# Kernel optimization log

Hardware: AMD Instinct MI355X
Metric: run time of the kernel (lower is better)

The kernel has to match this reference:

```python
import jax, jax.numpy as jnp
import numpy as np

NUM_LAYERS = 4
D_MODEL = 1024
N_HEAD = 8
HEAD_DIM = D_MODEL // N_HEAD
FFN_DIM = 4096
B, L = 8, 512
LN_EPS = 1e-5


def rel_pos_embed(seq_len, dim, init_size=1200, padding_idx=0):
    # RelativeSinusoidalPositionalEmbedding.get_embedding(init_size+1, dim, 0)
    num = init_size + 1  # 1201
    half = dim // 2
    inv = np.exp(np.arange(half, dtype=np.float64) * -(np.log(10000.0) / (half - 1)))
    pos = np.arange(-num // 2, num // 2, dtype=np.float64)[:, None] * inv[None, :]
    emb = np.concatenate([np.sin(pos), np.cos(pos)], axis=1)  # [num, dim]
    emb[padding_idx] = 0.0
    origin_shift = num // 2 + 1  # 601
    idx = np.arange(-seq_len, seq_len) + origin_shift  # [2L]
    return jnp.asarray(emb[idx], dtype=jnp.float32)  # [2L, dim]


def _shift(BD):
    # [b,h,L,2L] -> [b,h,L,L], selecting relative offsets k-q
    b, h, l, _ = BD.shape
    BD = jnp.concatenate([BD, jnp.zeros((b, h, l, 1), BD.dtype)], axis=-1)
    BD = BD.reshape(b, h, -1, l)[:, :, :-1].reshape(b, h, l, 2 * l)
    return BD[:, :, :, l:]


def _transpose_shift(E):
    # [b,h,L,2L] -> [b,h,L,L]
    b, h, l, _ = E.shape
    E = jnp.concatenate([E, jnp.zeros((b, h, l, 1), E.dtype)], axis=-1)
    E = E.reshape(b, h, 2 * l + 1, l)
    E = E[:, :, 2 * jnp.arange(l) + 1, :]  # [b,h,L,L]
    return jnp.swapaxes(E, -1, -2)


def layer_norm(x, g, b):
    mu = x.mean(-1, keepdims=True)
    var = ((x - mu) ** 2).mean(-1, keepdims=True)
    return (x - mu) / jnp.sqrt(var + LN_EPS) * g + b


def rel_attn(x, mask, qkv_w, r_r, r_w, pos):
    bsz, l, d = x.shape
    qkv = x @ qkv_w  # [b,L,3D]
    q, k, v = jnp.split(qkv, 3, axis=-1)
    to_heads = lambda t: t.reshape(bsz, l, N_HEAD, HEAD_DIM).transpose(0, 2, 1, 3)
    q, k, v = to_heads(q), to_heads(k), to_heads(v)  # [b,h,L,hd]
    rw_q = q + r_r[:, None]  # (original adds r_r_bias here)
    AC = jnp.einsum('bnqd,bnkd->bnqk', rw_q, k)
    D_ = jnp.einsum('nd,ld->nl', r_w, pos)[None, :, None]   # [1,h,1,2L]
    B_ = jnp.einsum('bnqd,ld->bnql', q, pos)                # [b,h,L,2L]
    E_ = jnp.einsum('bnqd,ld->bnql', k, pos)
    BDE = _shift(B_ + D_) + _transpose_shift(E_)
    attn = AC + BDE  # scale == 1 (scale=False)
    attn = jnp.where(mask[:, None, None, :] == 0, -jnp.inf, attn)
    attn = jax.nn.softmax(attn, axis=-1)
    out = jnp.einsum('bnqk,bnkd->bnqd', attn, v)
    return out.transpose(0, 2, 1, 3).reshape(bsz, l, d)


def setup_inputs() -> dict:
    key = jax.random.key(0)
    ks = jax.random.split(key, 12)
    Ln = NUM_LAYERS
    s = 0.02
    return {
        'x': jax.random.normal(ks[0], (B, L, D_MODEL), jnp.float32),
        'mask': jnp.ones((B, L), jnp.int32),
        'qkv_w': jax.random.normal(ks[1], (Ln, D_MODEL, 3 * D_MODEL), jnp.float32) * s,
        'r_r_bias': jax.random.normal(ks[2], (Ln, N_HEAD, HEAD_DIM), jnp.float32) * s,
        'r_w_bias': jax.random.normal(ks[3], (Ln, N_HEAD, HEAD_DIM), jnp.float32) * s,
        'ln1_g': jnp.ones((Ln, D_MODEL), jnp.float32),
        'ln1_b': jnp.zeros((Ln, D_MODEL), jnp.float32),
        'ln2_g': jnp.ones((Ln, D_MODEL), jnp.float32),
        'ln2_b': jnp.zeros((Ln, D_MODEL), jnp.float32),
        'w1': jax.random.normal(ks[4], (Ln, D_MODEL, FFN_DIM), jnp.float32) * s,
        'b1': jnp.zeros((Ln, FFN_DIM), jnp.float32),
        'w2': jax.random.normal(ks[5], (Ln, FFN_DIM, D_MODEL), jnp.float32) * s,
        'b2': jnp.zeros((Ln, D_MODEL), jnp.float32),
    }


def reference(x, mask, qkv_w, r_r_bias, r_w_bias, ln1_g, ln1_b, ln2_g, ln2_b, w1, b1, w2, b2):
    pos = rel_pos_embed(x.shape[1], HEAD_DIM)  # [2L, hd], buffer (detached)
    for i in range(NUM_LAYERS):  # after_norm=True (post-LN)
        a = rel_attn(x, mask, qkv_w[i], r_r_bias[i], r_w_bias[i], pos)
        x = layer_norm(x + a, ln1_g[i], ln1_b[i])
        h = jax.nn.relu(x @ w1[i] + b1[i]) @ w2[i] + b2[i]
        x = layer_norm(x + h, ln2_g[i], ln2_b[i])
    return x
```

## Files before the change

kernel.cpp:

```cpp
#include <hip/hip_runtime.h>

#define SEQ 512
#define DM 1024
#define NH 8
#define HD 128
#define FFN 4096
#define NL 4
#define NB 8

typedef __attribute__((ext_vector_type(8))) _Float16 half8v;
typedef __attribute__((ext_vector_type(8))) unsigned short ushort8v;
typedef __attribute__((ext_vector_type(4))) float float4v;

__device__ __forceinline__ unsigned short f2h(float f) {
  _Float16 h = (_Float16)f;
  return *(unsigned short*)&h;
}
__device__ __forceinline__ float h2f(unsigned short u) {
  _Float16 h = *(_Float16*)&u;
  return (float)h;
}

__global__ void sc_kernel(float* __restrict__ sc) {
  int idx = blockIdx.x * blockDim.x + threadIdx.x;
  int q = idx >> 6, c = idx & 63;
  if (q >= SEQ) return;
  double a = exp(-(double)c * (9.210340371976184 / 63.0));
  double p = (double)q * a;
  sc[q * 128 + c] = (float)sin(p);
  sc[q * 128 + 64 + c] = (float)cos(p);
}

__global__ void cvt_copy(const float* __restrict__ in, float* __restrict__ xout,
                         unsigned short* __restrict__ xh, int n4) {
  int i = blockIdx.x * blockDim.x + threadIdx.x;
  if (i >= n4) return;
  float4 v = ((const float4*)in)[i];
  ((float4*)xout)[i] = v;
  ushort4 u;
  u.x = f2h(v.x); u.y = f2h(v.y); u.z = f2h(v.z); u.w = f2h(v.w);
  ((ushort4*)xh)[i] = u;
}

__global__ __launch_bounds__(256) void transpose_cvt(
    const float* __restrict__ in, unsigned short* __restrict__ out, int K, int N) {
  __shared__ float t[32][33];
  int n0 = blockIdx.x * 32, k0 = blockIdx.y * 32;
  int c = threadIdx.x & 31, r = threadIdx.x >> 5;
#pragma unroll
  for (int i = 0; i < 32; i += 8)
    t[r + i][c] = in[(long long)(k0 + r + i) * N + n0 + c];
  __syncthreads();
#pragma unroll
  for (int i = 0; i < 32; i += 8)
    out[(long long)(n0 + r + i) * K + k0 + c] = f2h(t[c][r + i]);
}

template<int R>
__device__ __forceinline__ void stage_tile(
    const unsigned short* __restrict__ g, long long ld, int k0,
    unsigned short* lds, int tid) {
#pragma unroll
  for (int i = 0; i < R / 32; i++) {
    int p = i * 256 + tid;
    int row = p >> 3, cs = p & 7;
    int c = cs ^ (row & 7);
    const unsigned short* src = g + (long long)row * ld + k0 + c * 8;
    __builtin_amdgcn_global_load_lds(
        (const __attribute__((address_space(1))) void*)src,
        (__attribute__((address_space(3))) void*)(lds + p * 8),
        16, 0, 0);
  }
}

template<int BIAS, int RELU, int OUTH, int NF, int DBUF>
__global__ __launch_bounds__(256) void gemm_mfma(
    const unsigned short* __restrict__ A, int lda,
    const unsigned short* __restrict__ Bt, int ldb,
    const float* __restrict__ bias,
    void* __restrict__ Cv, int ldc,
    int K) {
  const int BN = 32 * NF;
  __shared__ __align__(16) unsigned short Asm[DBUF + 1][128 * 64];
  __shared__ __align__(16) unsigned short Bsm[DBUF + 1][BN * 64];
  const int tid = threadIdx.x, lane = tid & 63, wave = tid >> 6;
  const int wr = wave >> 1, wc = wave & 1;
  int nwg = gridDim.x * gridDim.y;
  int lin = blockIdx.y * gridDim.x + blockIdx.x;
  int swz = (lin & 7) * (nwg >> 3) + (lin >> 3);
  int bx = swz % gridDim.x, by = swz / gridDim.x;
  const unsigned short* Ag = A + (long long)by * 128 * lda;
  const unsigned short* Bg = Bt + (long long)bx * BN * ldb;
  const int l15 = lane & 15, l4 = lane >> 4;
  float4v acc[4][NF] = {};
  if (DBUF) {
    stage_tile<128>(Ag, lda, 0, Asm[0], tid);
    stage_tile<BN>(Bg, ldb, 0, Bsm[0], tid);
  }
  int cur = 0;
  for (int k0 = 0; k0 < K; k0 += 64) {
    if (DBUF) {
      __syncthreads();
      if (k0 + 64 < K) {
        stage_tile<128>(Ag, lda, k0 + 64, Asm[cur ^ 1], tid);
        stage_tile<BN>(Bg, ldb, k0 + 64, Bsm[cur ^ 1], tid);
      }
    } else {
      __syncthreads();
      stage_tile<128>(Ag, lda, k0, Asm[0], tid);
      stage_tile<BN>(Bg, ldb, k0, Bsm[0], tid);
      __syncthreads();
    }
#pragma unroll
    for (int kk = 0; kk < 2; kk++) {
      half8v af[4], bf[NF];
#pragma unroll
      for (int m = 0; m < 4; m++) {
        int row = wr * 64 + m * 16 + l15;
        int cs = (kk * 4 + l4) ^ (row & 7);
        af[m] = *(const half8v*)&Asm[cur][row * 64 + cs * 8];
      }
#pragma unroll
      for (int n = 0; n < NF; n++) {
        int row = wc * 16 * NF + n * 16 + l15;
        int cs = (kk * 4 + l4) ^ (row & 7);
        bf[n] = *(const half8v*)&Bsm[cur][row * 64 + cs * 8];
      }
#pragma unroll
      for (int m = 0; m < 4; m++)
#pragma unroll
        for (int n = 0; n < NF; n++)
          acc[m][n] = __builtin_amdgcn_mfma_f32_16x16x32_f16(af[m], bf[n], acc[m][n], 0, 0, 0);
    }
    if (DBUF) cur ^= 1;
  }
#pragma unroll
  for (int n = 0; n < NF; n++) {
    int ccol = bx * BN + wc * 16 * NF + n * 16 + l15;
    float bv = BIAS ? bias[ccol] : 0.f;
#pragma unroll
    for (int m = 0; m < 4; m++) {
      int crow0 = by * 128 + wr * 64 + m * 16 + l4 * 4;
#pragma unroll
      for (int j = 0; j < 4; j++) {
        float v = acc[m][n][j] + bv;
        if (RELU) v = fmaxf(v, 0.f);
        long long off = (long long)(crow0 + j) * ldc + ccol;
        if (OUTH) ((unsigned short*)Cv)[off] = f2h(v);
        else      ((float*)Cv)[off] = v;
      }
    }
  }
}

template<int OUTH, int ZSH, int NF, int DBUF>
__global__ __launch_bounds__(256) void gemm_bat(
    const unsigned short* __restrict__ A, int lda, long long sAz,
    const unsigned short* __restrict__ Bt, int ldb, long long sBz,
    void* __restrict__ Cv, int ldc, long long sCb, long long sCh,
    int K) {
  const int BN = 32 * NF;
  __shared__ __align__(16) unsigned short Asm[DBUF + 1][128 * 64];
  __shared__ __align__(16) unsigned short Bsm[DBUF + 1][BN * 64];
  const int tid = threadIdx.x, lane = tid & 63, wave = tid >> 6;
  const int wr = wave >> 1, wc = wave & 1;
  const int gx = gridDim.x, gy = gridDim.y;
  int nwg = gx * gy * gridDim.z;
  int lin = (blockIdx.z * gy + blockIdx.y) * gx + blockIdx.x;
  int swz = (lin & 7) * (nwg >> 3) + (lin >> 3);
  int bx = swz % gx;
  int t2 = swz / gx;
  int by = t2 % gy;
  int z  = t2 / gy;
  const int zb = z >> ZSH, zh = z & ((1 << ZSH) - 1);
  const unsigned short* Ag = A + (long long)z * sAz + (long long)by * 128 * lda;
  const unsigned short* Bg = Bt + (long long)z * sBz + (long long)bx * BN * ldb;
  const int l15 = lane & 15, l4 = lane >> 4;
  float4v acc[4][NF] = {};
  if (DBUF) {
    stage_tile<128>(Ag, lda, 0, Asm[0], tid);
    stage_tile<BN>(Bg, ldb, 0, Bsm[0], tid);
  }
  int cur = 0;
  for (int k0 = 0; k0 < K; k0 += 64) {
    if (DBUF) {
      __syncthreads();
      if (k0 + 64 < K) {
        stage_tile<128>(Ag, lda, k0 + 64, Asm[cur ^ 1], tid);
        stage_tile<BN>(Bg, ldb, k0 + 64, Bsm[cur ^ 1], tid);
      }
    } else {
      __syncthreads();
      stage_tile<128>(Ag, lda, k0, Asm[0], tid);
      stage_tile<BN>(Bg, ldb, k0, Bsm[0], tid);
      __syncthreads();
    }
#pragma unroll
    for (int kk = 0; kk < 2; kk++) {
      half8v af[4], bf[NF];
#pragma unroll
      for (int m = 0; m < 4; m++) {
        int row = wr * 64 + m * 16 + l15;
        int cs = (kk * 4 + l4) ^ (row & 7);
        af[m] = *(const half8v*)&Asm[cur][row * 64 + cs * 8];
      }
#pragma unroll
      for (int n = 0; n < NF; n++) {
        int row = wc * 16 * NF + n * 16 + l15;
        int cs = (kk * 4 + l4) ^ (row & 7);
        bf[n] = *(const half8v*)&Bsm[cur][row * 64 + cs * 8];
      }
#pragma unroll
      for (int m = 0; m < 4; m++)
#pragma unroll
        for (int n = 0; n < NF; n++)
          acc[m][n] = __builtin_amdgcn_mfma_f32_16x16x32_f16(af[m], bf[n], acc[m][n], 0, 0, 0);
    }
    if (DBUF) cur ^= 1;
  }
  long long cbase = (long long)zb * sCb + (long long)zh * sCh;
#pragma unroll
  for (int n = 0; n < NF; n++) {
    int ccol = bx * BN + wc * 16 * NF + n * 16 + l15;
#pragma unroll
    for (int m = 0; m < 4; m++) {
      int crow0 = by * 128 + wr * 64 + m * 16 + l4 * 4;
#pragma unroll
      for (int j = 0; j < 4; j++) {
        float v = acc[m][n][j];
        long long off = cbase + (long long)(crow0 + j) * ldc + ccol;
        if (OUTH) ((unsigned short*)Cv)[off] = f2h(v);
        else      ((float*)Cv)[off] = v;
      }
    }
  }
}

__global__ __launch_bounds__(256) void build_aug(
    const unsigned short* __restrict__ qkv_h,
    const float* __restrict__ rr, const float* __restrict__ rw,
    const float* __restrict__ sc,
    unsigned short* __restrict__ Ahat, unsigned short* __restrict__ Bhat)
{
  const int z = blockIdx.y, b = z >> 3, h = z & 7;
  const int r = threadIdx.x >> 7, lane = threadIdx.x & 127;
  const int q = blockIdx.x * 2 + r;
  __shared__ float Qf[2][128], Kf[2][128], SC[2][128];
  const unsigned short* row = qkv_h + ((long long)(b * SEQ + q)) * 3072 + h * HD;
  float qv = h2f(row[lane]);
  float kv = h2f(row[DM + lane]);
  Qf[r][lane] = qv + rw[h * HD + lane];
  Kf[r][lane] = kv;
  SC[r][lane] = sc[q * 128 + lane];
  __syncthreads();
  unsigned short* Arow = Ahat + ((long long)z * SEQ + q) * 384;
  unsigned short* Brow = Bhat + ((long long)z * SEQ + q) * 384;
  Arow[lane] = f2h(qv + rr[h * HD + lane]);
  Brow[lane] = f2h(kv);
  if (lane < 64) {
    float S = SC[r][lane], C = SC[r][64 + lane];
    Arow[128 + lane] = f2h(Qf[r][lane] * C + Qf[r][64 + lane] * S);
    Arow[256 + lane] = f2h(S);
    Brow[128 + lane] = f2h(S);
    Brow[256 + lane] = f2h(Kf[r][lane] * C + Kf[r][64 + lane] * S);
  } else {
    int c = lane - 64;
    float S = SC[r][c], C = SC[r][lane];
    Arow[192 + c] = f2h(Qf[r][lane] * C - Qf[r][c] * S);
    Arow[320 + c] = f2h(C);
    Brow[192 + c] = f2h(C);
    Brow[320 + c] = f2h(Kf[r][lane] * C - Kf[r][c] * S);
  }
}

__global__ __launch_bounds__(256) void transpose_v(
    const unsigned short* __restrict__ qkv_h, unsigned short* __restrict__ Vt)
{
  __shared__ unsigned short t[32][33];
  const int z = blockIdx.z, b = z >> 3, h = z & 7;
  const int d0 = blockIdx.x * 32, j0 = blockIdx.y * 32;
  const int c = threadIdx.x & 31, r = threadIdx.x >> 5;
#pragma unroll
  for (int i = 0; i < 32; i += 8)
    t[r + i][c] = qkv_h[((long long)(b * SEQ + j0 + r + i)) * 3072 + 2 * DM + h * HD + d0 + c];
  __syncthreads();
#pragma unroll
  for (int i = 0; i < 32; i += 8)
    Vt[(long long)z * HD * SEQ + (long long)(d0 + r + i) * SEQ + j0 + c] = t[c][r + i];
}

__global__ __launch_bounds__(256) void softmax_mask_h(
    unsigned short* __restrict__ scores16, const int* __restrict__ mask)
{
  const int z = blockIdx.y, b = z >> 3;
  const int wid = threadIdx.x >> 6, lane = threadIdx.x & 63;
  const int q = blockIdx.x * 4 + wid;
  unsigned short* row = scores16 + ((long long)z * SEQ + q) * SEQ;
  ushort8v u = ((ushort8v*)row)[lane];
  const int4* mp = (const int4*)(mask + (size_t)b * SEQ);
  int4 m0 = mp[lane * 2], m1 = mp[lane * 2 + 1];
  const int mk[8] = {m0.x, m0.y, m0.z, m0.w, m1.x, m1.y, m1.z, m1.w};
  float v[8];
  float mx = -1e30f;
#pragma unroll
  for (int i = 0; i < 8; i++) {
    v[i] = mk[i] ? h2f(u[i]) : -1e30f;
    mx = fmaxf(mx, v[i]);
  }
#pragma unroll
  for (int o = 32; o; o >>= 1) mx = fmaxf(mx, __shfl_xor(mx, o));
  float e[8], s = 0.f;
#pragma unroll
  for (int i = 0; i < 8; i++) { e[i] = __expf(v[i] - mx); s += e[i]; }
#pragma unroll
  for (int o = 32; o; o >>= 1) s += __shfl_xor(s, o);
  float inv = 1.f / s;
#pragma unroll
  for (int i = 0; i < 8; i++) u[i] = f2h(e[i] * inv);
  ((ushort8v*)row)[lane] = u;
}

__global__ __launch_bounds__(256) void add_ln_cvt(
    float* __restrict__ x, const unsigned short* __restrict__ a,
    const float* __restrict__ g, const float* __restrict__ bt,
    unsigned short* __restrict__ xh)
{
  const int row = blockIdx.x, tid = threadIdx.x;
  float4* xp = (float4*)(x + (size_t)row * DM);
  const ushort4 av = ((const ushort4*)(a + (size_t)row * DM))[tid];
  float4 xv = xp[tid];
  float4 s = make_float4(xv.x + h2f(av.x), xv.y + h2f(av.y),
                         xv.z + h2f(av.z), xv.w + h2f(av.w));
  __shared__ float red[4];
  float sum = s.x + s.y + s.z + s.w;
  for (int o = 32; o; o >>= 1) sum += __shfl_down(sum, o);
  if ((tid & 63) == 0) red[tid >> 6] = sum;
  __syncthreads();
  float mu = (red[0] + red[1] + red[2] + red[3]) * (1.f / DM);
  float dx = s.x - mu, dy = s.y - mu, dz = s.z - mu, dw = s.w - mu;
  float sq = dx * dx + dy * dy + dz * dz + dw * dw;
  for (int o = 32; o; o >>= 1) sq += __shfl_down(sq, o);
  __syncthreads();
  if ((tid & 63) == 0) red[tid >> 6] = sq;
  __syncthreads();
  float var = (red[0] + red[1] + red[2] + red[3]) * (1.f / DM);
  float rstd = rsqrtf(var + 1e-5f);
  const float4 gv = ((const float4*)g)[tid];
  const float4 bv = ((const float4*)bt)[tid];
  float4 o4 = make_float4(dx * rstd * gv.x + bv.x, dy * rstd * gv.y + bv.y,
                          dz * rstd * gv.z + bv.z, dw * rstd * gv.w + bv.w);
  xp[tid] = o4;
  ushort4 u;
  u.x = f2h(o4.x); u.y = f2h(o4.y); u.z = f2h(o4.z); u.w = f2h(o4.w);
  ((ushort4*)(xh + (size_t)row * DM))[tid] = u;
}

__global__ __launch_bounds__(256) void add_ln_cvt4(
    float* __restrict__ x, const float* __restrict__ p, long long pstride,
    const float* __restrict__ bias,
    const float* __restrict__ g, const float* __restrict__ bt,
    unsigned short* __restrict__ xh)
{
  const int row = blockIdx.x, tid = threadIdx.x;
  float4* xp = (float4*)(x + (size_t)row * DM);
  const float4 bb = ((const float4*)bias)[tid];
  float4 xv = xp[tid];
  float4 s = make_float4(xv.x + bb.x, xv.y + bb.y, xv.z + bb.z, xv.w + bb.w);
#pragma unroll
  for (int zz = 0; zz < 4; zz++) {
    const float4 a = ((const float4*)(p + zz * pstride + (size_t)row * DM))[tid];
    s.x += a.x; s.y += a.y; s.z += a.z; s.w += a.w;
  }
  __shared__ float red[4];
  float sum = s.x + s.y + s.z + s.w;
  for (int o = 32; o; o >>= 1) sum += __shfl_down(sum, o);
  if ((tid & 63) == 0) red[tid >> 6] = sum;
  __syncthreads();
  float mu = (red[0] + red[1] + red[2] + red[3]) * (1.f / DM);
  float dx = s.x - mu, dy = s.y - mu, dz = s.z - mu, dw = s.w - mu;
  float sq = dx * dx + dy * dy + dz * dz + dw * dw;
  for (int o = 32; o; o >>= 1) sq += __shfl_down(sq, o);
  __syncthreads();
  if ((tid & 63) == 0) red[tid >> 6] = sq;
  __syncthreads();
  float var = (red[0] + red[1] + red[2] + red[3]) * (1.f / DM);
  float rstd = rsqrtf(var + 1e-5f);
  const float4 gv = ((const float4*)g)[tid];
  const float4 bv = ((const float4*)bt)[tid];
  float4 o4 = make_float4(dx * rstd * gv.x + bv.x, dy * rstd * gv.y + bv.y,
                          dz * rstd * gv.z + bv.z, dw * rstd * gv.w + bv.w);
  xp[tid] = o4;
  ushort4 u;
  u.x = f2h(o4.x); u.y = f2h(o4.y); u.z = f2h(o4.z); u.w = f2h(o4.w);
  ((ushort4*)(xh + (size_t)row * DM))[tid] = u;
}

extern "C" void kernel_launch(void* const* d_in, const int* in_sizes, int n_in,
                              void* d_out, int out_size, void* d_ws, size_t ws_size,
                              hipStream_t stream)
{
  const float* x_in = (const float*)d_in[0];
  const int*   mask = (const int*)d_in[1];
  const float* qkv_w = (const float*)d_in[2];
  const float* r_r  = (const float*)d_in[3];
  const float* r_w  = (const float*)d_in[4];
  const float* ln1g = (const float*)d_in[5];
  const float* ln1b = (const float*)d_in[6];
  const float* ln2g = (const float*)d_in[7];
  const float* ln2b = (const float*)d_in[8];
  const float* w1   = (const float*)d_in[9];
  const float* b1   = (const float*)d_in[10];
  const float* w2   = (const float*)d_in[11];
  const float* b2   = (const float*)d_in[12];
  float* x = (float*)d_out;
  char* ws = (char*)d_ws;

  const int ROWS = NB * SEQ;

  const size_t sc_off   = 0;
  const size_t xh_off   = 0x40000;
  const size_t wt_off   = xh_off + (size_t)ROWS * DM * 2;
  const size_t a16_off  = wt_off + (size_t)FFN * DM * 2;
  const size_t qkvh_off = a16_off + (size_t)ROWS * DM * 2;
  const size_t e_off    = qkvh_off + (size_t)ROWS * 3 * DM * 2;

  const size_t hb_bytes = (size_t)ROWS * FFN * 2;
  const size_t part_off = e_off + hb_bytes;
  const size_t ffn_need = hb_bytes + 4 * (size_t)ROWS * DM * 4;

  int nb = 8;
  while (nb > 1) {
    size_t ab = (size_t)nb * 8 * SEQ * 384 * 2;
    size_t vt = (size_t)nb * 8 * HD * SEQ * 2;
    size_t scb = (size_t)nb * 8 * SEQ * SEQ * 2;
    size_t att_need = 2 * ab + vt + scb;
    size_t need = e_off + (att_need > ffn_need ? att_need : ffn_need);
    if (need <= ws_size) break;
    nb >>= 1;
  }
  const size_t ab_bytes = (size_t)nb * 8 * SEQ * 384 * 2;
  const size_t vt_bytes = (size_t)nb * 8 * HD * SEQ * 2;

  float* sc     = (float*)(ws + sc_off);
  unsigned short* xh = (unsigned short*)(ws + xh_off);
  unsigned short* wt = (unsigned short*)(ws + wt_off);
  unsigned short* a16 = (unsigned short*)(ws + a16_off);
  unsigned short* qkvh = (unsigned short*)(ws + qkvh_off);
  unsigned short* Ahat = (unsigned short*)(ws + e_off);
  unsigned short* Bhat = (unsigned short*)(ws + e_off + ab_bytes);
  unsigned short* Vt   = (unsigned short*)(ws + e_off + 2 * ab_bytes);
  unsigned short* scores16 = (unsigned short*)(ws + e_off + 2 * ab_bytes + vt_bytes);
  unsigned short* hb = (unsigned short*)(ws + e_off);
  float* part = (float*)(ws + part_off);

  sc_kernel<<<dim3(SEQ * 64 / 256), 256, 0, stream>>>(sc);
  cvt_copy<<<dim3(ROWS * DM / 4 / 256), 256, 0, stream>>>(x_in, x, xh, ROWS * DM / 4);

  for (int L = 0; L < NL; L++) {
    transpose_cvt<<<dim3(3 * DM / 32, DM / 32), 256, 0, stream>>>(
        qkv_w + (size_t)L * DM * 3 * DM, wt, DM, 3 * DM);
    gemm_mfma<0,0,1,4,0><<<dim3(3 * DM / 128, ROWS / 128), 256, 0, stream>>>(
        xh, DM, wt, DM, nullptr, qkvh, 3 * DM, DM);

    for (int b0 = 0; b0 < NB; b0 += nb) {
      const unsigned short* qkvh_b = qkvh + (size_t)b0 * SEQ * 3072;
      build_aug<<<dim3(SEQ / 2, nb * 8), 256, 0, stream>>>(
          qkvh_b, r_r + (size_t)L * NH * HD, r_w + (size_t)L * NH * HD, sc, Ahat, Bhat);
      transpose_v<<<dim3(HD / 32, SEQ / 32, nb * 8), 256, 0, stream>>>(qkvh_b, Vt);
      gemm_bat<1,0,4,0><<<dim3(SEQ / 128, SEQ / 128, nb * 8), 256, 0, stream>>>(
          Ahat, 384, (long long)SEQ * 384,
          Bhat, 384, (long long)SEQ * 384,
          scores16, SEQ, (long long)SEQ * SEQ, 0, 384);
      softmax_mask_h<<<dim3(SEQ / 4, nb * 8), 256, 0, stream>>>(scores16, mask + (size_t)b0 * SEQ);
      gemm_bat<1,3,2,1><<<dim3(HD / 64, SEQ / 128, nb * 8), 256, 0, stream>>>(
          scores16, SEQ, (long long)SEQ * SEQ,
          Vt, SEQ, (long long)HD * SEQ,
          a16 + (size_t)b0 * SEQ * DM, DM, (long long)SEQ * DM, HD, SEQ);
    }
    add_ln_cvt<<<dim3(ROWS), 256, 0, stream>>>(x, a16, ln1g + (size_t)L * DM, ln1b + (size_t)L * DM, xh);

    transpose_cvt<<<dim3(FFN / 32, DM / 32), 256, 0, stream>>>(
        w1 + (size_t)L * DM * FFN, wt, DM, FFN);
    gemm_mfma<1,1,1,4,0><<<dim3(FFN / 128, ROWS / 128), 256, 0, stream>>>(
        xh, DM, wt, DM, b1 + (size_t)L * FFN, hb, FFN, DM);

    transpose_cvt<<<dim3(DM / 32, FFN / 32), 256, 0, stream>>>(
        w2 + (size_t)L * FFN * DM, wt, FFN, DM);
    gemm_bat<0,0,4,0><<<dim3(DM / 128, ROWS / 128, 4), 256, 0, stream>>>(
        hb, FFN, 1024,
        wt, FFN, 1024,
        part, DM, (long long)ROWS * DM, 0, 1024);

    add_ln_cvt4<<<dim3(ROWS), 256, 0, stream>>>(
        x, part, (long long)ROWS * DM, b2 + (size_t)L * DM,
        ln2g + (size_t)L * DM, ln2b + (size_t)L * DM, xh);
  }
}
```

Measured before the change: 1.018 ms.

## Fuse score GEMM, masked softmax and PV GEMM into one attention kernel

Replaces the separate score GEMM, masked-softmax pass and PV GEMM with one kernel. Each workgroup computes a 64x512 score tile into LDS, applies the mask and exponentiation in place, then multiplies by V and normalises at write-out. This removes the fp16 score matrix round-trip through global memory and two launches per batch chunk. It also drops the workspace-size-driven batch chunking and always processes all 64 batch-head pairs at once. The cost is a large LDS footprint (about 80 KB per block), which limits occupancy, and a grid of only 512 workgroups.

```diff
diff --git a/kernel.cpp b/kernel.cpp
--- a/kernel.cpp
+++ b/kernel.cpp
@@ -289,35 +289,148 @@
     Vt[(long long)z * HD * SEQ + (long long)(d0 + r + i) * SEQ + j0 + c] = t[c][r + i];
 }
 
-__global__ __launch_bounds__(256) void softmax_mask_h(
-    unsigned short* __restrict__ scores16, const int* __restrict__ mask)
+__global__ __launch_bounds__(256) void attn_fused(
+    const unsigned short* __restrict__ Ahat,
+    const unsigned short* __restrict__ Bhat,
+    const unsigned short* __restrict__ Vt,
+    const int* __restrict__ mask,
+    unsigned short* __restrict__ out)
 {
-  const int z = blockIdx.y, b = z >> 3;
-  const int wid = threadIdx.x >> 6, lane = threadIdx.x & 63;
-  const int q = blockIdx.x * 4 + wid;
-  unsigned short* row = scores16 + ((long long)z * SEQ + q) * SEQ;
-  ushort8v u = ((ushort8v*)row)[lane];
-  const int4* mp = (const int4*)(mask + (size_t)b * SEQ);
-  int4 m0 = mp[lane * 2], m1 = mp[lane * 2 + 1];
-  const int mk[8] = {m0.x, m0.y, m0.z, m0.w, m1.x, m1.y, m1.z, m1.w};
-  float v[8];
-  float mx = -1e30f;
-#pragma unroll
-  for (int i = 0; i < 8; i++) {
-    v[i] = mk[i] ? h2f(u[i]) : -1e30f;
-    mx = fmaxf(mx, v[i]);
-  }
-#pragma unroll
-  for (int o = 32; o; o >>= 1) mx = fmaxf(mx, __shfl_xor(mx, o));
-  float e[8], s = 0.f;
-#pragma unroll
-  for (int i = 0; i < 8; i++) { e[i] = __expf(v[i] - mx); s += e[i]; }
-#pragma unroll
-  for (int o = 32; o; o >>= 1) s += __shfl_xor(s, o);
-  float inv = 1.f / s;
-#pragma unroll
-  for (int i = 0; i < 8; i++) u[i] = f2h(e[i] * inv);
-  ((ushort8v*)row)[lane] = u;
+  __shared__ __align__(16) unsigned short S[64 * 512];
+  __shared__ __align__(16) unsigned short St[16 * 512];
+  const int tid = threadIdx.x, lane = tid & 63, w = tid >> 6;
+  const int l15 = lane & 15, l4 = lane >> 4;
+  int lin = blockIdx.z * gridDim.x + blockIdx.x;
+  int nwg = gridDim.x * gridDim.z;
+  int swz = (lin & 7) * (nwg >> 3) + (lin >> 3);
+  int qt = swz % gridDim.x, z = swz / gridDim.x;
+  const int b = z >> 3, h = z & 7;
+  const int q0 = qt * 64;
+
+  half8v qf[12];
+  {
+    const unsigned short* Ar = Ahat + ((long long)z * SEQ + q0 + w * 16 + l15) * 384;
+#pragma unroll
+    for (int k = 0; k < 12; k++)
+      qf[k] = *(const half8v*)&Ar[k * 32 + l4 * 8];
+  }
+
+  for (int jt = 0; jt < 4; jt++) {
+    float4v acc[8] = {};
+    const unsigned short* Bg = Bhat + ((long long)z * SEQ + jt * 128) * 384;
+    for (int k0 = 0; k0 < 384; k0 += 64) {
+      __syncthreads();
+      stage_tile<128>(Bg, 384, k0, St, tid);
+      __syncthreads();
+#pragma unroll
+      for (int kk = 0; kk < 2; kk++) {
+        int kidx = (k0 >> 5) + kk;
+#pragma unroll
+        for (int n = 0; n < 8; n++) {
+          int row = n * 16 + l15;
+          int cs = (kk * 4 + l4) ^ (row & 7);
+          half8v bf = *(const half8v*)&St[row * 64 + cs * 8];
+          acc[n] = __builtin_amdgcn_mfma_f32_16x16x32_f16(qf[kidx], bf, acc[n], 0, 0, 0);
+        }
+      }
+    }
+#pragma unroll
+    for (int n = 0; n < 8; n++) {
+      int col = jt * 128 + n * 16 + l15;
+#pragma unroll
+      for (int j = 0; j < 4; j++) {
+        int row = w * 16 + l4 * 4 + j;
+        int byte = (row * 512 + col) * 2;
+        byte ^= (row & 7) << 4;
+        *(unsigned short*)((char*)S + byte) = f2h(acc[n][j]);
+      }
+    }
+  }
+  __syncthreads();
+
+  float* bias = (float*)St;
+  if (tid < 128) {
+    int4 mk = ((const int4*)(mask + (size_t)b * SEQ))[tid];
+    float4 bv;
+    bv.x = mk.x ? 0.f : -1e30f;
+    bv.y = mk.y ? 0.f : -1e30f;
+    bv.z = mk.z ? 0.f : -1e30f;
+    bv.w = mk.w ? 0.f : -1e30f;
+    ((float4*)bias)[tid] = bv;
+  }
+  __syncthreads();
+  float inv;
+  {
+    const int row = tid >> 2;
+    const int cb = (tid & 3) * 128;
+    ushort8v u[16];
+    int byt[16];
+#pragma unroll
+    for (int i = 0; i < 16; i++) {
+      int byte = (row * 512 + cb + i * 8) * 2;
+      byte ^= (row & 7) << 4;
+      byt[i] = byte;
+      u[i] = *(const ushort8v*)((const char*)S + byte);
+    }
+    float mx = -1e30f;
+#pragma unroll
+    for (int i = 0; i < 16; i++) {
+      const float* bp = bias + cb + i * 8;
+#pragma unroll
+      for (int e = 0; e < 8; e++)
+        mx = fmaxf(mx, h2f(u[i][e]) + bp[e]);
+    }
+    mx = fmaxf(mx, __shfl_xor(mx, 1));
+    mx = fmaxf(mx, __shfl_xor(mx, 2));
+    float sum = 0.f;
+#pragma unroll
+    for (int i = 0; i < 16; i++) {
+      const float* bp = bias + cb + i * 8;
+#pragma unroll
+      for (int e = 0; e < 8; e++) {
+        float ev = __expf(h2f(u[i][e]) + bp[e] - mx);
+        sum += ev;
+        u[i][e] = f2h(ev);
+      }
+      *(ushort8v*)((char*)S + byt[i]) = u[i];
+    }
+    sum += __shfl_xor(sum, 1);
+    sum += __shfl_xor(sum, 2);
+    inv = 1.f / sum;
+  }
+  __syncthreads();
+
+  float4v oacc[8] = {};
+  const unsigned short* Vg = Vt + (long long)z * HD * SEQ;
+  for (int k0 = 0; k0 < 512; k0 += 64) {
+    __syncthreads();
+    stage_tile<128>(Vg, 512, k0, St, tid);
+    __syncthreads();
+#pragma unroll
+    for (int kk = 0; kk < 2; kk++) {
+      int prow = w * 16 + l15;
+      int pb = (prow * 512 + k0 + kk * 32 + l4 * 8) * 2;
+      pb ^= (prow & 7) << 4;
+      half8v af = *(const half8v*)((const char*)S + pb);
+#pragma unroll
+      for (int n = 0; n < 8; n++) {
+        int row = n * 16 + l15;
+        int cs = (kk * 4 + l4) ^ (row & 7);
+        half8v bf = *(const half8v*)&St[row * 64 + cs * 8];
+        oacc[n] = __builtin_amdgcn_mfma_f32_16x16x32_f16(af, bf, oacc[n], 0, 0, 0);
+      }
+    }
+  }
+#pragma unroll
+  for (int j = 0; j < 4; j++) {
+    float rs = __shfl(inv, (l4 * 4 + j) * 4);
+    int row = q0 + w * 16 + l4 * 4 + j;
+#pragma unroll
+    for (int n = 0; n < 8; n++) {
+      int col = h * HD + n * 16 + l15;
+      out[((long long)(b * SEQ + row)) * DM + col] = f2h(oacc[n][j] * rs);
+    }
+  }
 }
 
 __global__ __launch_bounds__(256) void add_ln_cvt(
@@ -424,22 +537,9 @@
   const size_t qkvh_off = a16_off + (size_t)ROWS * DM * 2;
   const size_t e_off    = qkvh_off + (size_t)ROWS * 3 * DM * 2;
 
+  const size_t ab_bytes = (size_t)64 * SEQ * 384 * 2;
   const size_t hb_bytes = (size_t)ROWS * FFN * 2;
   const size_t part_off = e_off + hb_bytes;
-  const size_t ffn_need = hb_bytes + 4 * (size_t)ROWS * DM * 4;
-
-  int nb = 8;
-  while (nb > 1) {
-    size_t ab = (size_t)nb * 8 * SEQ * 384 * 2;
-    size_t vt = (size_t)nb * 8 * HD * SEQ * 2;
-    size_t scb = (size_t)nb * 8 * SEQ * SEQ * 2;
-    size_t att_need = 2 * ab + vt + scb;
-    size_t need = e_off + (att_need > ffn_need ? att_need : ffn_need);
-    if (need <= ws_size) break;
-    nb >>= 1;
-  }
-  const size_t ab_bytes = (size_t)nb * 8 * SEQ * 384 * 2;
-  const size_t vt_bytes = (size_t)nb * 8 * HD * SEQ * 2;
 
   float* sc     = (float*)(ws + sc_off);
   unsigned short* xh = (unsigned short*)(ws + xh_off);
@@ -449,7 +549,6 @@
   unsigned short* Ahat = (unsigned short*)(ws + e_off);
   unsigned short* Bhat = (unsigned short*)(ws + e_off + ab_bytes);
   unsigned short* Vt   = (unsigned short*)(ws + e_off + 2 * ab_bytes);
-  unsigned short* scores16 = (unsigned short*)(ws + e_off + 2 * ab_bytes + vt_bytes);
   unsigned short* hb = (unsigned short*)(ws + e_off);
   float* part = (float*)(ws + part_off);
 
@@ -462,21 +561,11 @@
     gemm_mfma<0,0,1,4,0><<<dim3(3 * DM / 128, ROWS / 128), 256, 0, stream>>>(
         xh, DM, wt, DM, nullptr, qkvh, 3 * DM, DM);
 
-    for (int b0 = 0; b0 < NB; b0 += nb) {
-      const unsigned short* qkvh_b = qkvh + (size_t)b0 * SEQ * 3072;
-      build_aug<<<dim3(SEQ / 2, nb * 8), 256, 0, stream>>>(
-          qkvh_b, r_r + (size_t)L * NH * HD, r_w + (size_t)L * NH * HD, sc, Ahat, Bhat);
-      transpose_v<<<dim3(HD / 32, SEQ / 32, nb * 8), 256, 0, stream>>>(qkvh_b, Vt);
-      gemm_bat<1,0,4,0><<<dim3(SEQ / 128, SEQ / 128, nb * 8), 256, 0, stream>>>(
-          Ahat, 384, (long long)SEQ * 384,
-          Bhat, 384, (long long)SEQ * 384,
-          scores16, SEQ, (long long)SEQ * SEQ, 0, 384);
-      softmax_mask_h<<<dim3(SEQ / 4, nb * 8), 256, 0, stream>>>(scores16, mask + (size_t)b0 * SEQ);
-      gemm_bat<1,3,2,1><<<dim3(HD / 64, SEQ / 128, nb * 8), 256, 0, stream>>>(
-          scores16, SEQ, (long long)SEQ * SEQ,
-          Vt, SEQ, (long long)HD * SEQ,
-          a16 + (size_t)b0 * SEQ * DM, DM, (long long)SEQ * DM, HD, SEQ);
-    }
+    build_aug<<<dim3(SEQ / 2, 64), 256, 0, stream>>>(
+        qkvh, r_r + (size_t)L * NH * HD, r_w + (size_t)L * NH * HD, sc, Ahat, Bhat);
+    transpose_v<<<dim3(HD / 32, SEQ / 32, 64), 256, 0, stream>>>(qkvh, Vt);
+    attn_fused<<<dim3(SEQ / 64, 1, 64), 256, 0, stream>>>(Ahat, Bhat, Vt, mask, a16);
+
     add_ln_cvt<<<dim3(ROWS), 256, 0, stream>>>(x, a16, ln1g + (size_t)L * DM, ln1b + (size_t)L * DM, xh);
 
     transpose_cvt<<<dim3(FFN / 32, DM / 32), 256, 0, stream>>>(
```

After: 1.076 ms. 1.06x slower.
